# Performance work log

Measured on AMD Instinct MI355X. Metric: run time of the kernel, lower is better.

Reference implementation:

```python
import jax, jax.numpy as jnp
import numpy as np
import math

D_MODEL = 1024
N_HEADS = 16
HEAD_DIM = D_MODEL // N_HEADS

def setup_inputs() -> dict:
    key = jax.random.key(0)
    k1, k2, k3 = jax.random.split(key, 3)
    B, T = 4, 2048
    x = jax.random.normal(k1, (B, T, D_MODEL), dtype=jnp.float32)
    # weights stored as [in, out]; equivalent to torch Linear weight.T
    w_qkv = jax.random.normal(k2, (D_MODEL, 3 * D_MODEL), dtype=jnp.float32) * (1.0 / math.sqrt(D_MODEL))
    w_proj = jax.random.normal(k3, (D_MODEL, D_MODEL), dtype=jnp.float32) * (1.0 / math.sqrt(D_MODEL))
    return {"x": x, "w_qkv": w_qkv, "w_proj": w_proj}

def reference(x, w_qkv, w_proj):
    B, T, C = x.shape
    qkv = x @ w_qkv  # [B,T,3C]
    q, k, v = jnp.split(qkv, 3, axis=-1)
    # [B,T,C] -> [B,H,T,Dh]
    def to_heads(t):
        return t.reshape(B, T, N_HEADS, HEAD_DIM).transpose(0, 2, 1, 3)
    q, k, v = to_heads(q), to_heads(k), to_heads(v)
    scale = 1.0 / math.sqrt(HEAD_DIM)
    att = jnp.einsum('bhqd,bhkd->bhqk', q, k) * scale  # [B,H,T,T]
    causal = jnp.tril(jnp.ones((T, T), dtype=bool))
    att = jnp.where(causal[None, None], att, -jnp.inf)
    att = jax.nn.softmax(att, axis=-1)
    y = jnp.einsum('bhqk,bhkd->bhqd', att, v)  # [B,H,T,Dh]
    y = y.transpose(0, 2, 1, 3).reshape(B, T, C)
    return y @ w_proj
```

## Files before the change

### kernel.cpp

```cpp
#include <hip/hip_runtime.h>
#include <hip/hip_bf16.h>

typedef __bf16 bf16x8 __attribute__((ext_vector_type(8)));
typedef __bf16 bf16x4 __attribute__((ext_vector_type(4)));
typedef float  f32x4  __attribute__((ext_vector_type(4)));

#define MFMA16(a,b,c) __builtin_amdgcn_mfma_f32_16x16x32_bf16((a),(b),(c),0,0,0)

#define T_SEQ 2048
#define CDIM  1024
#define NH    16
#define DH    64
#define C3    3072

#define GLDS(g, l) __builtin_amdgcn_global_load_lds( \
    (const __attribute__((address_space(1))) void*)(g), \
    (__attribute__((address_space(3))) void*)(l), 16, 0, 0)

__global__ void cast_f32_bf16_kernel(const float* __restrict__ in,
                                     __bf16* __restrict__ out, int n4) {
  int i = blockIdx.x * 256 + threadIdx.x;
  if (i >= n4) return;
  f32x4 v = ((const f32x4*)in)[i];
  bf16x4 o;
  o[0] = (__bf16)v[0]; o[1] = (__bf16)v[1];
  o[2] = (__bf16)v[2]; o[3] = (__bf16)v[3];
  ((bf16x4*)out)[i] = o;
}

__global__ void transpose_cast_kernel(const float* __restrict__ W,
                                      __bf16* __restrict__ WT, int R, int C,
                                      float qscale, int qcols) {
  __shared__ float tile[32][33];
  int c0 = blockIdx.x * 32, r0 = blockIdx.y * 32;
  int tx = threadIdx.x, ty = threadIdx.y;
#pragma unroll
  for (int i = 0; i < 32; i += 8)
    tile[ty + i][tx] = W[(size_t)(r0 + ty + i) * C + c0 + tx];
  __syncthreads();
#pragma unroll
  for (int i = 0; i < 32; i += 8) {
    int c = c0 + ty + i;
    float sc = (c < qcols) ? qscale : 1.0f;
    WT[(size_t)c * R + r0 + tx] = (__bf16)(tile[tx][ty + i] * sc);
  }
}

__global__ void transpose_v_kernel(const __bf16* __restrict__ qkv,
                                   __bf16* __restrict__ VT) {
  __shared__ __bf16 tile[64][65];
  int b  = blockIdx.z;
  int t0 = blockIdx.x * 64;
  int c0 = blockIdx.y * 64;
  int tx = threadIdx.x & 63;
  int ty = threadIdx.x >> 6;
#pragma unroll
  for (int i = 0; i < 64; i += 4)
    tile[ty + i][tx] = qkv[(size_t)(b * T_SEQ + t0 + ty + i) * C3 + 2 * CDIM + c0 + tx];
  __syncthreads();
#pragma unroll
  for (int i = 0; i < 64; i += 4)
    VT[((size_t)b * CDIM + c0 + ty + i) * T_SEQ + t0 + tx] = tile[tx][ty + i];
}

template <int STORE_BF16>
__global__ __launch_bounds__(512, 1)
void gemm256_kernel(const __bf16* __restrict__ A, const __bf16* __restrict__ BT,
                    void* __restrict__ Cout, int M, int N, int K, int nbm) {
  __shared__ __align__(16) __bf16 S[2][2][2][128 * 64];
  const int tid  = threadIdx.x;
  const int lane = tid & 63;
  const int g    = lane >> 4;
  const int l16  = lane & 15;
  const int wave = tid >> 6;
  const int wm   = wave >> 2;
  const int wn   = wave & 3;

  const int nwg = gridDim.x;
  const int sb  = (blockIdx.x & 7) * (nwg >> 3) + (blockIdx.x >> 3);
  const int bm  = sb % nbm;
  const int bn  = sb / nbm;

  const int srow = tid >> 3;
  const int scol = ((tid & 7) << 4) ^ ((srow & 7) << 4);
  const int swz  = (l16 & 7) << 4;

  const __bf16* Abase = A  + (size_t)(bm * 256 + srow) * K + (scol >> 1);
  const __bf16* Bbase = BT + (size_t)(bn * 256 + srow) * K + (scol >> 1);

  f32x4  acc[8][4] = {};
  bf16x8 ar[4][2];
  bf16x8 br[2][2][2];

#define STAGE(BUF, H, K0) do { \
    const __bf16* sp_ = ((H) < 2 ? Abase : Bbase) + (size_t)((H) & 1) * 128 * K + (K0); \
    char* dp_ = (char*)&S[BUF][(H) >> 1][(H) & 1][0] + tid * 16; \
    GLDS(sp_, dp_); \
    GLDS(sp_ + (size_t)64 * K, dp_ + 8192); \
  } while (0)

#define LDA(BUF, MH) do { \
    const char* ab_ = (const char*)&S[BUF][0][wm][0]; \
    _Pragma("unroll") for (int i_ = 0; i_ < 4; ++i_) { \
      const char* rp_ = ab_ + ((MH) * 64 + i_ * 16 + l16) * 128; \
      _Pragma("unroll") for (int kk_ = 0; kk_ < 2; ++kk_) \
        ar[i_][kk_] = *(const bf16x8*)(rp_ + ((kk_ * 64 + g * 16) ^ swz)); \
    } \
  } while (0)

#define LDB(BUF, NHF) do { \
    const char* bb_ = (const char*)&S[BUF][1][wn >> 1][0]; \
    _Pragma("unroll") for (int j_ = 0; j_ < 2; ++j_) { \
      const char* rp_ = bb_ + ((wn & 1) * 64 + ((NHF) * 2 + j_) * 16 + l16) * 128; \
      _Pragma("unroll") for (int kk_ = 0; kk_ < 2; ++kk_) \
        br[NHF][j_][kk_] = *(const bf16x8*)(rp_ + ((kk_ * 64 + g * 16) ^ swz)); \
    } \
  } while (0)

#define MQUAD(MH, NHF) do { \
    __builtin_amdgcn_s_setprio(1); \
    _Pragma("unroll") for (int i_ = 0; i_ < 4; ++i_) \
      _Pragma("unroll") for (int j_ = 0; j_ < 2; ++j_) \
        _Pragma("unroll") for (int kk_ = 0; kk_ < 2; ++kk_) \
          acc[(MH) * 4 + i_][(NHF) * 2 + j_] = \
              MFMA16(ar[i_][kk_], br[NHF][j_][kk_], acc[(MH) * 4 + i_][(NHF) * 2 + j_]); \
    __builtin_amdgcn_s_setprio(0); \
  } while (0)

#define SBAR do { \
    __builtin_amdgcn_sched_barrier(0); \
    __builtin_amdgcn_s_barrier(); \
    __builtin_amdgcn_sched_barrier(0); \
  } while (0)

  STAGE(0, 0, 0); STAGE(0, 1, 0); STAGE(0, 2, 0); STAGE(0, 3, 0);
  STAGE(1, 0, 64);
  asm volatile("s_waitcnt vmcnt(2)" ::: "memory");
  SBAR;

  const int NIT = K >> 7;
#pragma unroll 1
  for (int it = 0; it < NIT; ++it) {
    const int k1 = (2 * it + 1) << 6;
    const int k2 = (2 * it + 2) << 6;
    const int k3 = (2 * it + 3) << 6;
    const bool stg = (it + 1) < NIT;

    LDA(0, 0); LDB(0, 0);
    STAGE(1, 1, k1);
    SBAR; MQUAD(0, 0); SBAR;
    LDB(0, 1);
    STAGE(1, 2, k1);
    SBAR; MQUAD(0, 1); SBAR;
    LDA(0, 1);
    STAGE(1, 3, k1);
    SBAR; MQUAD(1, 1); SBAR;
    if (stg) { STAGE(0, 0, k2); asm volatile("s_waitcnt vmcnt(2)" ::: "memory"); }
    else     { asm volatile("s_waitcnt vmcnt(0)" ::: "memory"); }
    SBAR; MQUAD(1, 0); SBAR;

    LDA(1, 0); LDB(1, 0);
    if (stg) STAGE(0, 1, k2);
    SBAR; MQUAD(0, 0); SBAR;
    LDB(1, 1);
    if (stg) STAGE(0, 2, k2);
    SBAR; MQUAD(0, 1); SBAR;
    LDA(1, 1);
    if (stg) STAGE(0, 3, k2);
    SBAR; MQUAD(1, 1); SBAR;
    if (stg) { STAGE(1, 0, k3); asm volatile("s_waitcnt vmcnt(2)" ::: "memory"); }
    SBAR; MQUAD(1, 0); SBAR;
  }

#pragma unroll
  for (int ii = 0; ii < 8; ++ii) {
    const int row0 = bm * 256 + wm * 128 + ii * 16 + g * 4;
#pragma unroll
    for (int jj = 0; jj < 4; ++jj) {
      const int col = bn * 256 + wn * 64 + jj * 16 + l16;
#pragma unroll
      for (int r = 0; r < 4; ++r) {
        size_t idx = (size_t)(row0 + r) * N + col;
        if (STORE_BF16) ((__bf16*)Cout)[idx] = (__bf16)acc[ii][jj][r];
        else            ((float*)Cout)[idx]  = acc[ii][jj][r];
      }
    }
  }
#undef STAGE
#undef LDA
#undef LDB
#undef MQUAD
#undef SBAR
}

__global__ __launch_bounds__(256)
void attn_kernel(const __bf16* __restrict__ qkv, const __bf16* __restrict__ VT,
                 __bf16* __restrict__ y) {
  __shared__ __align__(16) __bf16 Klds[2][64 * 64];
  __shared__ __align__(16) __bf16 Vlds[2][64 * 64];
  __shared__ __align__(16) __bf16 Plds[4][32 * 64];
  const int tid  = threadIdx.x;
  const int lane = tid & 63;
  const int g    = lane >> 4;
  const int l16  = lane & 15;
  const int wave = tid >> 6;

  const int pairid = blockIdx.x >> 6;
  const int bh     = blockIdx.x & 63;
  const int h      = bh & (NH - 1);
  const int b      = bh >> 4;

  const __bf16* Qg = qkv + (size_t)b * T_SEQ * C3 + h * DH;
  const __bf16* Kg = Qg + CDIM;
  const __bf16* Vt = VT + ((size_t)b * CDIM + h * DH) * T_SEQ;

  const int srow = tid >> 3;
  const int scol = ((tid & 7) * 16) ^ ((srow & 7) << 4);
  const int swz  = (l16 & 7) << 4;

  const float NEG = -3.0e38f;

  bf16x8 ones;
#pragma unroll
  for (int j = 0; j < 8; ++j) ones[j] = (__bf16)1.0f;

  char* Pw = (char*)&Plds[wave][0];

#pragma unroll 1
  for (int ph = 0; ph < 2; ++ph) {
    const int qt    = ph ? (15 - pairid) : pairid;
    const int qbase = qt * 128 + wave * 32;

    bf16x8 qf[2][2];
#pragma unroll
    for (int qg = 0; qg < 2; ++qg)
#pragma unroll
      for (int kk = 0; kk < 2; ++kk)
        qf[qg][kk] = *(const bf16x8*)(Qg + (size_t)(qbase + qg * 16 + l16) * C3 + kk * 32 + g * 8);

    f32x4 o[2][4] = {};
    f32x4 o_l[2]  = {};

    const int nkb = 2 * qt + 2;
    {
      const __bf16* ksrc = Kg + (size_t)srow * C3 + (scol >> 1);
      GLDS(ksrc, (char*)&Klds[0][0] + tid * 16);
      GLDS(ksrc + (size_t)32 * C3, (char*)&Klds[0][0] + 4096 + tid * 16);
      const __bf16* vsrc = Vt + (size_t)srow * T_SEQ + (scol >> 1);
      GLDS(vsrc, (char*)&Vlds[0][0] + tid * 16);
      GLDS(vsrc + (size_t)32 * T_SEQ, (char*)&Vlds[0][0] + 4096 + tid * 16);
    }
    __syncthreads();

    const __bf16* kstage = Kg + (size_t)(64 + srow) * C3 + (scol >> 1);
    const __bf16* vstage = Vt + (size_t)srow * T_SEQ + 64 + (scol >> 1);

#pragma unroll 1
    for (int kb = 0; kb < nkb; ++kb) {
      const int cur = kb & 1;
      if (kb + 1 < nkb) {
        GLDS(kstage, (char*)&Klds[cur ^ 1][0] + tid * 16);
        GLDS(kstage + (size_t)32 * C3, (char*)&Klds[cur ^ 1][0] + 4096 + tid * 16);
        GLDS(vstage, (char*)&Vlds[cur ^ 1][0] + tid * 16);
        GLDS(vstage + (size_t)32 * T_SEQ, (char*)&Vlds[cur ^ 1][0] + 4096 + tid * 16);
        kstage += (size_t)64 * C3;
        vstage += 64;
      }

      f32x4 s[2][4] = {};
      const char* Kb = (const char*)&Klds[cur][0];
#pragma unroll
      for (int st = 0; st < 4; ++st) {
        const char* rowp = Kb + (st * 16 + l16) * 128;
#pragma unroll
        for (int kk = 0; kk < 2; ++kk) {
          bf16x8 kf = *(const bf16x8*)(rowp + ((kk * 64 + g * 16) ^ swz));
          s[0][st] = MFMA16(kf, qf[0][kk], s[0][st]);
          s[1][st] = MFMA16(kf, qf[1][kk], s[1][st]);
        }
      }
      if (kb >= 2 * qt) {
        const int kvbase = (kb - 2 * qt) * 64;
#pragma unroll
        for (int qg = 0; qg < 2; ++qg) {
          const int qloc = wave * 32 + qg * 16 + l16;
#pragma unroll
          for (int st = 0; st < 4; ++st)
#pragma unroll
            for (int r = 0; r < 4; ++r)
              if (kvbase + st * 16 + g * 4 + r > qloc) s[qg][st][r] = NEG;
        }
      }
#pragma unroll
      for (int qg = 0; qg < 2; ++qg) {
        char* Pr = Pw + (qg * 16 + l16) * 128;
#pragma unroll
        for (int st = 0; st < 4; ++st) {
          bf16x4 pb;
#pragma unroll
          for (int r = 0; r < 4; ++r)
            pb[r] = (__bf16)__builtin_amdgcn_exp2f(s[qg][st][r]);
          *(bf16x4*)(Pr + ((st * 32 + g * 8) ^ swz)) = pb;
        }
      }

      const char* Vb = (const char*)&Vlds[cur][0];
#pragma unroll
      for (int hf = 0; hf < 2; ++hf) {
        bf16x8 pf0 = *(const bf16x8*)(Pw + (l16)       * 128 + ((hf * 64 + g * 16) ^ swz));
        bf16x8 pf1 = *(const bf16x8*)(Pw + (16 + l16)  * 128 + ((hf * 64 + g * 16) ^ swz));
        o_l[0] = MFMA16(ones, pf0, o_l[0]);
        o_l[1] = MFMA16(ones, pf1, o_l[1]);
#pragma unroll
        for (int dt = 0; dt < 4; ++dt) {
          bf16x8 vf = *(const bf16x8*)(Vb + (dt * 16 + l16) * 128 + ((hf * 64 + g * 16) ^ swz));
          o[0][dt] = MFMA16(vf, pf0, o[0][dt]);
          o[1][dt] = MFMA16(vf, pf1, o[1][dt]);
        }
      }
      __syncthreads();
    }

#pragma unroll
    for (int qg = 0; qg < 2; ++qg) {
      const float inv_l = 1.0f / o_l[qg][0];
      const int qrow = qbase + qg * 16 + l16;
#pragma unroll
      for (int dt = 0; dt < 4; ++dt)
#pragma unroll
        for (int r = 0; r < 4; ++r)
          y[((size_t)b * T_SEQ + qrow) * CDIM + h * DH + dt * 16 + g * 4 + r] =
              (__bf16)(o[qg][dt][r] * inv_l);
    }
  }
}

extern "C" void kernel_launch(void* const* d_in, const int* in_sizes, int n_in,
                              void* d_out, int out_size, void* d_ws, size_t ws_size,
                              hipStream_t stream) {
  const float* x      = (const float*)d_in[0];
  const float* w_qkv  = (const float*)d_in[1];
  const float* w_proj = (const float*)d_in[2];
  float* out = (float*)d_out;

  __bf16* xb     = (__bf16*)d_ws;
  __bf16* wqkvT  = xb + 8388608;
  __bf16* wprojT = wqkvT + 3145728;
  __bf16* qkv    = wprojT + 1048576;
  __bf16* yb     = qkv + 25165824;
  __bf16* VT     = xb;

  const float SCF = 0.125f * 1.44269504088896340736f;

  cast_f32_bf16_kernel<<<8192, 256, 0, stream>>>(x, xb, 2097152);
  transpose_cast_kernel<<<dim3(96, 32), dim3(32, 8), 0, stream>>>(w_qkv, wqkvT, 1024, 3072, SCF, 1024);
  transpose_cast_kernel<<<dim3(32, 32), dim3(32, 8), 0, stream>>>(w_proj, wprojT, 1024, 1024, 1.0f, 0);
  gemm256_kernel<1><<<384, 512, 0, stream>>>(xb, wqkvT, (void*)qkv, 8192, 3072, 1024, 32);
  transpose_v_kernel<<<dim3(32, 16, 4), 256, 0, stream>>>(qkv, VT);
  attn_kernel<<<512, 256, 0, stream>>>(qkv, VT, yb);
  gemm256_kernel<0><<<128, 512, 0, stream>>>(yb, wprojT, (void*)out, 8192, 1024, 1024, 32);
}
```

Measured before the change: 180.7 us.

## Shrink GEMM tile to 256x128 with triple-buffered LDS pipeline

Changes the GEMM block tile from 256x256 to 256x128, which doubles the grid (768 and 256 workgroups) so the 256 CUs are better filled, especially for the projection GEMM that previously launched only 128 blocks. The K loop now steps one 64-wide slice at a time over a three-stage LDS ring buffer, issuing loads two slices ahead with adjusted vmcnt waits. The cost is lower arithmetic intensity per block, since each A tile is reused across fewer columns, and more total global/L2 traffic.

```diff
diff --git a/kernel.cpp b/kernel.cpp
--- a/kernel.cpp
+++ b/kernel.cpp
@@ -67,7 +67,7 @@
 __global__ __launch_bounds__(512, 1)
 void gemm256_kernel(const __bf16* __restrict__ A, const __bf16* __restrict__ BT,
                     void* __restrict__ Cout, int M, int N, int K, int nbm) {
-  __shared__ __align__(16) __bf16 S[2][2][2][128 * 64];
+  __shared__ __align__(16) __bf16 S[3][3][128 * 64];
   const int tid  = threadIdx.x;
   const int lane = tid & 63;
   const int g    = lane >> 4;
@@ -86,21 +86,21 @@
   const int swz  = (l16 & 7) << 4;
 
   const __bf16* Abase = A  + (size_t)(bm * 256 + srow) * K + (scol >> 1);
-  const __bf16* Bbase = BT + (size_t)(bn * 256 + srow) * K + (scol >> 1);
-
-  f32x4  acc[8][4] = {};
+  const __bf16* Bbase = BT + (size_t)(bn * 128 + srow) * K + (scol >> 1);
+
+  f32x4  acc[8][2] = {};
   bf16x8 ar[4][2];
-  bf16x8 br[2][2][2];
-
-#define STAGE(BUF, H, K0) do { \
-    const __bf16* sp_ = ((H) < 2 ? Abase : Bbase) + (size_t)((H) & 1) * 128 * K + (K0); \
-    char* dp_ = (char*)&S[BUF][(H) >> 1][(H) & 1][0] + tid * 16; \
+  bf16x8 br[2][2];
+
+#define STAGE(BUF, U, K0) do { \
+    const __bf16* sp_ = ((U) < 2 ? Abase + (size_t)(U) * 128 * K : Bbase) + (K0); \
+    char* dp_ = (char*)&S[BUF][U][0] + tid * 16; \
     GLDS(sp_, dp_); \
     GLDS(sp_ + (size_t)64 * K, dp_ + 8192); \
   } while (0)
 
 #define LDA(BUF, MH) do { \
-    const char* ab_ = (const char*)&S[BUF][0][wm][0]; \
+    const char* ab_ = (const char*)&S[BUF][wm][0]; \
     _Pragma("unroll") for (int i_ = 0; i_ < 4; ++i_) { \
       const char* rp_ = ab_ + ((MH) * 64 + i_ * 16 + l16) * 128; \
       _Pragma("unroll") for (int kk_ = 0; kk_ < 2; ++kk_) \
@@ -108,22 +108,22 @@
     } \
   } while (0)
 
-#define LDB(BUF, NHF) do { \
-    const char* bb_ = (const char*)&S[BUF][1][wn >> 1][0]; \
+#define LDB(BUF) do { \
+    const char* bb_ = (const char*)&S[BUF][2][0]; \
     _Pragma("unroll") for (int j_ = 0; j_ < 2; ++j_) { \
-      const char* rp_ = bb_ + ((wn & 1) * 64 + ((NHF) * 2 + j_) * 16 + l16) * 128; \
+      const char* rp_ = bb_ + (wn * 32 + j_ * 16 + l16) * 128; \
       _Pragma("unroll") for (int kk_ = 0; kk_ < 2; ++kk_) \
-        br[NHF][j_][kk_] = *(const bf16x8*)(rp_ + ((kk_ * 64 + g * 16) ^ swz)); \
+        br[j_][kk_] = *(const bf16x8*)(rp_ + ((kk_ * 64 + g * 16) ^ swz)); \
     } \
   } while (0)
 
-#define MQUAD(MH, NHF) do { \
+#define MQUAD(MH) do { \
     __builtin_amdgcn_s_setprio(1); \
     _Pragma("unroll") for (int i_ = 0; i_ < 4; ++i_) \
       _Pragma("unroll") for (int j_ = 0; j_ < 2; ++j_) \
         _Pragma("unroll") for (int kk_ = 0; kk_ < 2; ++kk_) \
-          acc[(MH) * 4 + i_][(NHF) * 2 + j_] = \
-              MFMA16(ar[i_][kk_], br[NHF][j_][kk_], acc[(MH) * 4 + i_][(NHF) * 2 + j_]); \
+          acc[(MH) * 4 + i_][j_] = \
+              MFMA16(ar[i_][kk_], br[j_][kk_], acc[(MH) * 4 + i_][j_]); \
     __builtin_amdgcn_s_setprio(0); \
   } while (0)
 
@@ -133,51 +133,41 @@
     __builtin_amdgcn_sched_barrier(0); \
   } while (0)
 
-  STAGE(0, 0, 0); STAGE(0, 1, 0); STAGE(0, 2, 0); STAGE(0, 3, 0);
-  STAGE(1, 0, 64);
-  asm volatile("s_waitcnt vmcnt(2)" ::: "memory");
+  STAGE(0, 0, 0);  STAGE(0, 1, 0);  STAGE(0, 2, 0);
+  STAGE(1, 0, 64); STAGE(1, 1, 64); STAGE(1, 2, 64);
+  asm volatile("s_waitcnt vmcnt(6)" ::: "memory");
   SBAR;
 
-  const int NIT = K >> 7;
+  const int NT = K >> 6;
+  int js = 0, ws = 2;
 #pragma unroll 1
-  for (int it = 0; it < NIT; ++it) {
-    const int k1 = (2 * it + 1) << 6;
-    const int k2 = (2 * it + 2) << 6;
-    const int k3 = (2 * it + 3) << 6;
-    const bool stg = (it + 1) < NIT;
-
-    LDA(0, 0); LDB(0, 0);
-    STAGE(1, 1, k1);
-    SBAR; MQUAD(0, 0); SBAR;
-    LDB(0, 1);
-    STAGE(1, 2, k1);
-    SBAR; MQUAD(0, 1); SBAR;
-    LDA(0, 1);
-    STAGE(1, 3, k1);
-    SBAR; MQUAD(1, 1); SBAR;
-    if (stg) { STAGE(0, 0, k2); asm volatile("s_waitcnt vmcnt(2)" ::: "memory"); }
-    else     { asm volatile("s_waitcnt vmcnt(0)" ::: "memory"); }
-    SBAR; MQUAD(1, 0); SBAR;
-
-    LDA(1, 0); LDB(1, 0);
-    if (stg) STAGE(0, 1, k2);
-    SBAR; MQUAD(0, 0); SBAR;
-    LDB(1, 1);
-    if (stg) STAGE(0, 2, k2);
-    SBAR; MQUAD(0, 1); SBAR;
-    LDA(1, 1);
-    if (stg) STAGE(0, 3, k2);
-    SBAR; MQUAD(1, 1); SBAR;
-    if (stg) { STAGE(1, 0, k3); asm volatile("s_waitcnt vmcnt(2)" ::: "memory"); }
-    SBAR; MQUAD(1, 0); SBAR;
+  for (int j = 0; j < NT; ++j) {
+    const bool stg = (j + 2) < NT;
+    const int  k2  = (j + 2) << 6;
+
+    LDA(js, 0); LDB(js);
+    if (stg) { STAGE(ws, 0, k2); asm volatile("s_waitcnt vmcnt(8)" ::: "memory"); }
+    SBAR; MQUAD(0); SBAR;
+
+    LDA(js, 1);
+    if (stg) {
+      STAGE(ws, 1, k2); STAGE(ws, 2, k2);
+      asm volatile("s_waitcnt vmcnt(6)" ::: "memory");
+    } else if (j + 1 < NT) {
+      asm volatile("s_waitcnt vmcnt(0)" ::: "memory");
+    }
+    SBAR; MQUAD(1); SBAR;
+
+    js = (js == 2) ? 0 : js + 1;
+    ws = (ws == 2) ? 0 : ws + 1;
   }
 
 #pragma unroll
   for (int ii = 0; ii < 8; ++ii) {
     const int row0 = bm * 256 + wm * 128 + ii * 16 + g * 4;
 #pragma unroll
-    for (int jj = 0; jj < 4; ++jj) {
-      const int col = bn * 256 + wn * 64 + jj * 16 + l16;
+    for (int jj = 0; jj < 2; ++jj) {
+      const int col = bn * 128 + wn * 32 + jj * 16 + l16;
 #pragma unroll
       for (int r = 0; r < 4; ++r) {
         size_t idx = (size_t)(row0 + r) * N + col;
@@ -355,8 +345,8 @@
   cast_f32_bf16_kernel<<<8192, 256, 0, stream>>>(x, xb, 2097152);
   transpose_cast_kernel<<<dim3(96, 32), dim3(32, 8), 0, stream>>>(w_qkv, wqkvT, 1024, 3072, SCF, 1024);
   transpose_cast_kernel<<<dim3(32, 32), dim3(32, 8), 0, stream>>>(w_proj, wprojT, 1024, 1024, 1.0f, 0);
-  gemm256_kernel<1><<<384, 512, 0, stream>>>(xb, wqkvT, (void*)qkv, 8192, 3072, 1024, 32);
+  gemm256_kernel<1><<<768, 512, 0, stream>>>(xb, wqkvT, (void*)qkv, 8192, 3072, 1024, 32);
   transpose_v_kernel<<<dim3(32, 16, 4), 256, 0, stream>>>(qkv, VT);
   attn_kernel<<<512, 256, 0, stream>>>(qkv, VT, yb);
-  gemm256_kernel<0><<<128, 512, 0, stream>>>(yb, wprojT, (void*)out, 8192, 1024, 1024, 32);
-}
+  gemm256_kernel<0><<<256, 512, 0, stream>>>(yb, wprojT, (void*)out, 8192, 1024, 1024, 32);
+}
```

After: 186.8 us. +3.4%, slower.

## Split GEMM tile staging into half-tiles and reschedule loads for deeper prefetch

Applied to the files above, without the earlier changes.

Splits the LDS staging macro into 64-row half-tile loads and reorders them so that the quarter-tiles not yet read are prefetched earlier in the k-loop. More direct global-to-LDS loads are in flight at once, and the waitcnt thresholds change from 2 to 6. The aim is to hide global memory latency better behind the MFMA phases. The tradeoff is a more intricate hazard ordering: a buffer region must not be overwritten while waves are still reading it.

```diff
diff --git a/kernel.cpp b/kernel.cpp
--- a/kernel.cpp
+++ b/kernel.cpp
@@ -92,11 +92,10 @@
   bf16x8 ar[4][2];
   bf16x8 br[2][2][2];
 
-#define STAGE(BUF, H, K0) do { \
-    const __bf16* sp_ = ((H) < 2 ? Abase : Bbase) + (size_t)((H) & 1) * 128 * K + (K0); \
-    char* dp_ = (char*)&S[BUF][(H) >> 1][(H) & 1][0] + tid * 16; \
-    GLDS(sp_, dp_); \
-    GLDS(sp_ + (size_t)64 * K, dp_ + 8192); \
+#define STAGE1(BUF, H, SUB, K0) do { \
+    const __bf16* sp_ = ((H) < 2 ? Abase : Bbase) + \
+        (size_t)(((H) & 1) * 128 + (SUB) * 64) * K + (K0); \
+    GLDS(sp_, (char*)&S[BUF][(H) >> 1][(H) & 1][0] + (SUB) * 8192 + tid * 16); \
   } while (0)
 
 #define LDA(BUF, MH) do { \
@@ -133,9 +132,11 @@
     __builtin_amdgcn_sched_barrier(0); \
   } while (0)
 
-  STAGE(0, 0, 0); STAGE(0, 1, 0); STAGE(0, 2, 0); STAGE(0, 3, 0);
-  STAGE(1, 0, 64);
-  asm volatile("s_waitcnt vmcnt(2)" ::: "memory");
+  STAGE1(0, 0, 0, 0); STAGE1(0, 0, 1, 0); STAGE1(0, 1, 0, 0); STAGE1(0, 1, 1, 0);
+  STAGE1(0, 2, 0, 0); STAGE1(0, 2, 1, 0); STAGE1(0, 3, 0, 0); STAGE1(0, 3, 1, 0);
+  STAGE1(1, 0, 0, 64); STAGE1(1, 1, 0, 64);
+  STAGE1(1, 2, 0, 64); STAGE1(1, 2, 1, 64); STAGE1(1, 3, 0, 64); STAGE1(1, 3, 1, 64);
+  asm volatile("s_waitcnt vmcnt(6)" ::: "memory");
   SBAR;
 
   const int NIT = K >> 7;
@@ -147,28 +148,35 @@
     const bool stg = (it + 1) < NIT;
 
     LDA(0, 0); LDB(0, 0);
-    STAGE(1, 1, k1);
+    STAGE1(1, 0, 1, k1); STAGE1(1, 1, 1, k1);
     SBAR; MQUAD(0, 0); SBAR;
     LDB(0, 1);
-    STAGE(1, 2, k1);
+    if (stg) { STAGE1(0, 0, 0, k2); STAGE1(0, 1, 0, k2); }
     SBAR; MQUAD(0, 1); SBAR;
     LDA(0, 1);
-    STAGE(1, 3, k1);
+    if (stg) { STAGE1(0, 2, 0, k2); STAGE1(0, 2, 1, k2); }
     SBAR; MQUAD(1, 1); SBAR;
-    if (stg) { STAGE(0, 0, k2); asm volatile("s_waitcnt vmcnt(2)" ::: "memory"); }
-    else     { asm volatile("s_waitcnt vmcnt(0)" ::: "memory"); }
+    if (stg) {
+      STAGE1(0, 3, 0, k2); STAGE1(0, 3, 1, k2);
+      asm volatile("s_waitcnt vmcnt(6)" ::: "memory");
+    } else {
+      asm volatile("s_waitcnt vmcnt(0)" ::: "memory");
+    }
     SBAR; MQUAD(1, 0); SBAR;
 
     LDA(1, 0); LDB(1, 0);
-    if (stg) STAGE(0, 1, k2);
+    if (stg) { STAGE1(0, 0, 1, k2); STAGE1(0, 1, 1, k2); }
     SBAR; MQUAD(0, 0); SBAR;
     LDB(1, 1);
-    if (stg) STAGE(0, 2, k2);
+    if (stg) { STAGE1(1, 0, 0, k3); STAGE1(1, 1, 0, k3); }
     SBAR; MQUAD(0, 1); SBAR;
     LDA(1, 1);
-    if (stg) STAGE(0, 3, k2);
+    if (stg) { STAGE1(1, 2, 0, k3); STAGE1(1, 2, 1, k3); }
     SBAR; MQUAD(1, 1); SBAR;
-    if (stg) { STAGE(1, 0, k3); asm volatile("s_waitcnt vmcnt(2)" ::: "memory"); }
+    if (stg) {
+      STAGE1(1, 3, 0, k3); STAGE1(1, 3, 1, k3);
+      asm volatile("s_waitcnt vmcnt(6)" ::: "memory");
+    }
     SBAR; MQUAD(1, 0); SBAR;
   }
 
@@ -186,7 +194,7 @@
       }
     }
   }
-#undef STAGE
+#undef STAGE1
 #undef LDA
 #undef LDB
 #undef MQUAD
```

New measurement: 182.9 us. Within noise of the previous version (+1.3%).

## Fuse V transpose into QKV GEMM epilogue and drop separate transpose kernel

Applied to the files above, without the earlier changes.

The QKV GEMM epilogue now writes Q and K to a compact 2048-wide buffer and writes V directly transposed into the VT layout, so the standalone transpose_v kernel and its extra read/write pass over V go away. The attention kernel reads Q/K from the narrower buffer. The block-to-tile mapping also changes from M-major to N-major ordering, which alters L2 reuse patterns. The V-transposed stores are 8-byte strided scatters, which may be less coalesced than the old row stores.

```diff
diff --git a/kernel.cpp b/kernel.cpp
--- a/kernel.cpp
+++ b/kernel.cpp
@@ -12,6 +12,7 @@
 #define NH    16
 #define DH    64
 #define C3    3072
+#define QKS   2048
 
 #define GLDS(g, l) __builtin_amdgcn_global_load_lds( \
     (const __attribute__((address_space(1))) void*)(g), \
@@ -46,27 +47,11 @@
   }
 }
 
-__global__ void transpose_v_kernel(const __bf16* __restrict__ qkv,
-                                   __bf16* __restrict__ VT) {
-  __shared__ __bf16 tile[64][65];
-  int b  = blockIdx.z;
-  int t0 = blockIdx.x * 64;
-  int c0 = blockIdx.y * 64;
-  int tx = threadIdx.x & 63;
-  int ty = threadIdx.x >> 6;
-#pragma unroll
-  for (int i = 0; i < 64; i += 4)
-    tile[ty + i][tx] = qkv[(size_t)(b * T_SEQ + t0 + ty + i) * C3 + 2 * CDIM + c0 + tx];
-  __syncthreads();
-#pragma unroll
-  for (int i = 0; i < 64; i += 4)
-    VT[((size_t)b * CDIM + c0 + ty + i) * T_SEQ + t0 + tx] = tile[tx][ty + i];
-}
-
-template <int STORE_BF16>
+template <int MODE>
 __global__ __launch_bounds__(512, 1)
 void gemm256_kernel(const __bf16* __restrict__ A, const __bf16* __restrict__ BT,
-                    void* __restrict__ Cout, int M, int N, int K, int nbm) {
+                    void* __restrict__ Cout, __bf16* __restrict__ VTp,
+                    int K, int nbn) {
   __shared__ __align__(16) __bf16 S[2][2][2][128 * 64];
   const int tid  = threadIdx.x;
   const int lane = tid & 63;
@@ -78,8 +63,8 @@
 
   const int nwg = gridDim.x;
   const int sb  = (blockIdx.x & 7) * (nwg >> 3) + (blockIdx.x >> 3);
-  const int bm  = sb % nbm;
-  const int bn  = sb / nbm;
+  const int bn  = sb % nbn;
+  const int bm  = sb / nbn;
 
   const int srow = tid >> 3;
   const int scol = ((tid & 7) << 4) ^ ((srow & 7) << 4);
@@ -172,17 +157,43 @@
     SBAR; MQUAD(1, 0); SBAR;
   }
 
-#pragma unroll
-  for (int ii = 0; ii < 8; ++ii) {
-    const int row0 = bm * 256 + wm * 128 + ii * 16 + g * 4;
-#pragma unroll
-    for (int jj = 0; jj < 4; ++jj) {
-      const int col = bn * 256 + wn * 64 + jj * 16 + l16;
-#pragma unroll
-      for (int r = 0; r < 4; ++r) {
-        size_t idx = (size_t)(row0 + r) * N + col;
-        if (STORE_BF16) ((__bf16*)Cout)[idx] = (__bf16)acc[ii][jj][r];
-        else            ((float*)Cout)[idx]  = acc[ii][jj][r];
+  if (MODE == 0) {
+#pragma unroll
+    for (int ii = 0; ii < 8; ++ii) {
+      const int row0 = bm * 256 + wm * 128 + ii * 16 + g * 4;
+#pragma unroll
+      for (int jj = 0; jj < 4; ++jj) {
+        const int col = bn * 256 + wn * 64 + jj * 16 + l16;
+#pragma unroll
+        for (int r = 0; r < 4; ++r)
+          ((float*)Cout)[(size_t)(row0 + r) * 1024 + col] = acc[ii][jj][r];
+      }
+    }
+  } else if (bn < 8) {
+#pragma unroll
+    for (int ii = 0; ii < 8; ++ii) {
+      const int row0 = bm * 256 + wm * 128 + ii * 16 + g * 4;
+#pragma unroll
+      for (int jj = 0; jj < 4; ++jj) {
+        const int col = bn * 256 + wn * 64 + jj * 16 + l16;
+#pragma unroll
+        for (int r = 0; r < 4; ++r)
+          ((__bf16*)Cout)[(size_t)(row0 + r) * QKS + col] = (__bf16)acc[ii][jj][r];
+      }
+    }
+  } else {
+#pragma unroll
+    for (int ii = 0; ii < 8; ++ii) {
+      const int row0 = bm * 256 + wm * 128 + ii * 16 + g * 4;
+      const int b    = row0 >> 11;
+      const int t0   = row0 & 2047;
+#pragma unroll
+      for (int jj = 0; jj < 4; ++jj) {
+        const int c = (bn - 8) * 256 + wn * 64 + jj * 16 + l16;
+        bf16x4 pb;
+#pragma unroll
+        for (int r = 0; r < 4; ++r) pb[r] = (__bf16)acc[ii][jj][r];
+        *(bf16x4*)(VTp + ((size_t)((b << 10) + c)) * T_SEQ + t0) = pb;
       }
     }
   }
@@ -194,7 +205,7 @@
 }
 
 __global__ __launch_bounds__(256)
-void attn_kernel(const __bf16* __restrict__ qkv, const __bf16* __restrict__ VT,
+void attn_kernel(const __bf16* __restrict__ qk, const __bf16* __restrict__ VT,
                  __bf16* __restrict__ y) {
   __shared__ __align__(16) __bf16 Klds[2][64 * 64];
   __shared__ __align__(16) __bf16 Vlds[2][64 * 64];
@@ -210,9 +221,9 @@
   const int h      = bh & (NH - 1);
   const int b      = bh >> 4;
 
-  const __bf16* Qg = qkv + (size_t)b * T_SEQ * C3 + h * DH;
-  const __bf16* Kg = Qg + CDIM;
-  const __bf16* Vt = VT + ((size_t)b * CDIM + h * DH) * T_SEQ;
+  const __bf16* Qg = qk + (size_t)b * T_SEQ * QKS + h * DH;
+  const __bf16* Kg = Qg + 1024;
+  const __bf16* Vt = VT + ((size_t)(b << 10) + h * DH) * T_SEQ;
 
   const int srow = tid >> 3;
   const int scol = ((tid & 7) * 16) ^ ((srow & 7) << 4);
@@ -236,23 +247,23 @@
     for (int qg = 0; qg < 2; ++qg)
 #pragma unroll
       for (int kk = 0; kk < 2; ++kk)
-        qf[qg][kk] = *(const bf16x8*)(Qg + (size_t)(qbase + qg * 16 + l16) * C3 + kk * 32 + g * 8);
+        qf[qg][kk] = *(const bf16x8*)(Qg + (size_t)(qbase + qg * 16 + l16) * QKS + kk * 32 + g * 8);
 
     f32x4 o[2][4] = {};
     f32x4 o_l[2]  = {};
 
     const int nkb = 2 * qt + 2;
     {
-      const __bf16* ksrc = Kg + (size_t)srow * C3 + (scol >> 1);
+      const __bf16* ksrc = Kg + (size_t)srow * QKS + (scol >> 1);
       GLDS(ksrc, (char*)&Klds[0][0] + tid * 16);
-      GLDS(ksrc + (size_t)32 * C3, (char*)&Klds[0][0] + 4096 + tid * 16);
+      GLDS(ksrc + (size_t)32 * QKS, (char*)&Klds[0][0] + 4096 + tid * 16);
       const __bf16* vsrc = Vt + (size_t)srow * T_SEQ + (scol >> 1);
       GLDS(vsrc, (char*)&Vlds[0][0] + tid * 16);
       GLDS(vsrc + (size_t)32 * T_SEQ, (char*)&Vlds[0][0] + 4096 + tid * 16);
     }
     __syncthreads();
 
-    const __bf16* kstage = Kg + (size_t)(64 + srow) * C3 + (scol >> 1);
+    const __bf16* kstage = Kg + (size_t)(64 + srow) * QKS + (scol >> 1);
     const __bf16* vstage = Vt + (size_t)srow * T_SEQ + 64 + (scol >> 1);
 
 #pragma unroll 1
@@ -260,10 +271,10 @@
       const int cur = kb & 1;
       if (kb + 1 < nkb) {
         GLDS(kstage, (char*)&Klds[cur ^ 1][0] + tid * 16);
-        GLDS(kstage + (size_t)32 * C3, (char*)&Klds[cur ^ 1][0] + 4096 + tid * 16);
+        GLDS(kstage + (size_t)32 * QKS, (char*)&Klds[cur ^ 1][0] + 4096 + tid * 16);
         GLDS(vstage, (char*)&Vlds[cur ^ 1][0] + tid * 16);
         GLDS(vstage + (size_t)32 * T_SEQ, (char*)&Vlds[cur ^ 1][0] + 4096 + tid * 16);
-        kstage += (size_t)64 * C3;
+        kstage += (size_t)64 * QKS;
         vstage += 64;
       }
 
@@ -346,17 +357,16 @@
   __bf16* xb     = (__bf16*)d_ws;
   __bf16* wqkvT  = xb + 8388608;
   __bf16* wprojT = wqkvT + 3145728;
-  __bf16* qkv    = wprojT + 1048576;
-  __bf16* yb     = qkv + 25165824;
-  __bf16* VT     = xb;
+  __bf16* qk     = wprojT + 1048576;
+  __bf16* VT     = qk + 16777216;
+  __bf16* yb     = VT + 8388608;
 
   const float SCF = 0.125f * 1.44269504088896340736f;
 
   cast_f32_bf16_kernel<<<8192, 256, 0, stream>>>(x, xb, 2097152);
   transpose_cast_kernel<<<dim3(96, 32), dim3(32, 8), 0, stream>>>(w_qkv, wqkvT, 1024, 3072, SCF, 1024);
   transpose_cast_kernel<<<dim3(32, 32), dim3(32, 8), 0, stream>>>(w_proj, wprojT, 1024, 1024, 1.0f, 0);
-  gemm256_kernel<1><<<384, 512, 0, stream>>>(xb, wqkvT, (void*)qkv, 8192, 3072, 1024, 32);
-  transpose_v_kernel<<<dim3(32, 16, 4), 256, 0, stream>>>(qkv, VT);
-  attn_kernel<<<512, 256, 0, stream>>>(qkv, VT, yb);
-  gemm256_kernel<0><<<128, 512, 0, stream>>>(yb, wprojT, (void*)out, 8192, 1024, 1024, 32);
-}
+  gemm256_kernel<1><<<384, 512, 0, stream>>>(xb, wqkvT, (void*)qk, VT, 1024, 12);
+  attn_kernel<<<512, 256, 0, stream>>>(qk, VT, yb);
+  gemm256_kernel<0><<<128, 512, 0, stream>>>(yb, wprojT, (void*)out, nullptr, 1024, 4);
+}
```

After: 174.6 us. 3.3% less time.
